# Kernel tuning notes

Hardware: AMD Instinct MI355X
Metric: run time of the kernel (lower is better)

The kernel has to match this reference:

```python
import jax, jax.numpy as jnp
import numpy as np

T, B, NIN = 256, 256, 512
NH, NEMB = 512, 256


def setup_inputs() -> dict:
    key = jax.random.key(0)
    ks = jax.random.split(key, 11)
    s = 0.02  # small init to keep tanh/sigmoid in active range
    return {
        "feats": jax.random.normal(ks[0], (T, B, NIN), jnp.float32),
        "h": jax.random.normal(ks[1], (B, NH), jnp.float32),
        "cur_embed": jax.random.normal(ks[2], (B, NEMB), jnp.float32),
        # i2h: Linear(nIn, nHidden, bias=False)
        "w_i2h": jax.random.normal(ks[3], (NH, NIN), jnp.float32) * s,
        # h2h: Linear(nHidden, nHidden) with bias
        "w_h2h": jax.random.normal(ks[4], (NH, NH), jnp.float32) * s,
        "b_h2h": jax.random.normal(ks[5], (NH,), jnp.float32) * s,
        # score: Linear(nHidden, 1, bias=False)
        "w_score": jax.random.normal(ks[6], (NH,), jnp.float32) * s,
        # GRUCell(nIn + num_embeddings, nHidden); gate order r, z, n
        "w_ih": jax.random.normal(ks[7], (3 * NH, NIN + NEMB), jnp.float32) * s,
        "w_hh": jax.random.normal(ks[8], (3 * NH, NH), jnp.float32) * s,
        "b_ih": jax.random.normal(ks[9], (3 * NH,), jnp.float32) * s,
        "b_hh": jax.random.normal(ks[10], (3 * NH,), jnp.float32) * s,
    }


def reference(feats, h, cur_embed, w_i2h, w_h2h, b_h2h, w_score,
              w_ih, w_hh, b_ih, b_hh):
    # MORAN branch, test=True (FractionalPickup is skipped at eval time).
    # feats: [T, B, nIn], h: [B, nHidden], cur_embed: [B, nEmb]
    feats_ = jnp.einsum('tbc,hc->tbh', feats, w_i2h)          # i2h, [T,B,H]
    h_ = h @ w_h2h.T + b_h2h                                   # h2h, [B,H]
    emit = jnp.einsum('tbh,h->tb', jnp.tanh(feats_ + h_[None]), w_score)
    alpha = jax.nn.softmax(emit, axis=0)                       # softmax over T
    context = jnp.einsum('tb,tbc->bc', alpha, feats)           # [B,nIn]
    x = jnp.concatenate([context, cur_embed], axis=1)          # [B,nIn+nEmb]
    # GRUCell
    gi = x @ w_ih.T + b_ih                                     # [B,3H]
    gh = h @ w_hh.T + b_hh                                     # [B,3H]
    gi_r, gi_z, gi_n = jnp.split(gi, 3, axis=1)
    gh_r, gh_z, gh_n = jnp.split(gh, 3, axis=1)
    r = jax.nn.sigmoid(gi_r + gh_r)
    z = jax.nn.sigmoid(gi_z + gh_z)
    n = jnp.tanh(gi_n + r * gh_n)
    nh = (1.0 - z) * n + z * h
    return nh, alpha
```

## Files before the change

kernel.cpp:

```cpp
#include <hip/hip_runtime.h>

typedef __bf16 bf16;
typedef __bf16 bf16x4 __attribute__((ext_vector_type(4)));
typedef __bf16 bf16x8 __attribute__((ext_vector_type(8)));
typedef float  f32x4  __attribute__((ext_vector_type(4)));

#define T_DIM 256
#define B_DIM 256
#define NIN   512
#define NH    512
#define NEMB  256
#define NX    768
#define NG    1536

__device__ __forceinline__ float fast_tanh(float x) {
    float e = __expf(2.0f * x);
    return 1.0f - 2.0f * __builtin_amdgcn_rcpf(e + 1.0f);
}
__device__ __forceinline__ float fast_sigmoid(float x) {
    return __builtin_amdgcn_rcpf(1.0f + __expf(-x));
}

__device__ __forceinline__ int swz(int rc) { return ((rc >> 1) & 3) << 3; }

__global__ __launch_bounds__(256) void cvt_weights(
    const float* __restrict__ a0, const float* __restrict__ a1,
    const float* __restrict__ a2, const float* __restrict__ a3,
    const float* __restrict__ a4,
    bf16* __restrict__ b0, bf16* __restrict__ b1, bf16* __restrict__ b2,
    bf16* __restrict__ b3, bf16* __restrict__ b4) {
    const int N0 = 65536, N1 = 131072, N2 = 425984, N3 = 622592, N4 = 655360;
    for (int i = blockIdx.x * 256 + threadIdx.x; i < N4; i += gridDim.x * 256) {
        const float* s; bf16* d; int j; bool img = false;
        if (i < N0)      { s = a0; d = b0; j = i; img = true; }
        else if (i < N1) { s = a1; d = b1; j = i - N0; }
        else if (i < N2) { s = a2; d = b2; j = i - N1; }
        else if (i < N3) { s = a3; d = b3; j = i - N2; }
        else             { s = a4; d = b4; j = i - N3; }
        float4 v = reinterpret_cast<const float4*>(s)[j];
        bf16x4 o = { (bf16)v.x, (bf16)v.y, (bf16)v.z, (bf16)v.w };
        if (img) {
            int e = j * 4, col = e >> 9, kc = e & 511, kk = kc >> 5, k = kc & 31;
            int off = kk * 16384 + col * 32 + (k ^ swz(col));
            *reinterpret_cast<bf16x4*>(d + off) = o;
        } else {
            reinterpret_cast<bf16x4*>(d)[j] = o;
        }
    }
}

__global__ __launch_bounds__(256) void gemm_bias(
    const bf16* __restrict__ A, const bf16* __restrict__ B,
    const float* __restrict__ bias, float* __restrict__ C,
    int M, int N, int K) {
    __shared__ bf16 At[64][40];
    __shared__ bf16 Bt[64][40];
    const int tid = threadIdx.x;
    const int m0 = blockIdx.y * 64, n0 = blockIdx.x * 64;
    const int wid = tid >> 6, lane = tid & 63, hi = lane >> 4, lo = lane & 15;
    const int srow = tid >> 2, sseg = tid & 3;
    f32x4 acc[4] = {};

    for (int kk = 0; kk < K; kk += 32) {
        bf16x8 av = *reinterpret_cast<const bf16x8*>(A + (size_t)(m0 + srow) * K + kk + sseg * 8);
        bf16x8 bv = *reinterpret_cast<const bf16x8*>(B + (size_t)(n0 + srow) * K + kk + sseg * 8);
        __syncthreads();
        *reinterpret_cast<bf16x8*>(&At[srow][sseg * 8]) = av;
        *reinterpret_cast<bf16x8*>(&Bt[srow][sseg * 8]) = bv;
        __syncthreads();
        bf16x8 a = *reinterpret_cast<const bf16x8*>(&At[wid * 16 + lo][hi * 8]);
#pragma unroll
        for (int nt = 0; nt < 4; ++nt) {
            bf16x8 b = *reinterpret_cast<const bf16x8*>(&Bt[nt * 16 + lo][hi * 8]);
            acc[nt] = __builtin_amdgcn_mfma_f32_16x16x32_bf16(a, b, acc[nt], 0, 0, 0);
        }
    }
#pragma unroll
    for (int nt = 0; nt < 4; ++nt) {
        int n = n0 + nt * 16 + lo;
        float bv = bias[n];
#pragma unroll
        for (int r = 0; r < 4; ++r) {
            int m = m0 + wid * 16 + hi * 4 + r;
            C[(size_t)m * N + n] = acc[nt][r] + bv;
        }
    }
}

__global__ __launch_bounds__(512, 2) void emit_kernel(
    const float* __restrict__ feats, const bf16* __restrict__ Wimg,
    const float* __restrict__ hbuf, const float* __restrict__ wscore,
    float* __restrict__ emit_out) {
    __shared__ bf16 Atile[2][2048];
    __shared__ float ew[512];
    const int tid = threadIdx.x;
    const int m0 = blockIdx.x * 64;
    const int wid = tid >> 6, lane = tid & 63, hi = lane >> 4, lo = lane & 15;

    const int arow = tid >> 3, akq = tid & 7;
    const int aoff = arow * 32 + ((akq * 4) ^ swz(arow));
    const float* asrc = feats + (size_t)(m0 + arow) * NIN + akq * 4;

    const int col0 = wid * 64 + lo;
    const bf16* bsrc = Wimg + col0 * 32 + ((hi * 8) ^ swz(col0));

    float4 fa[3];
    bf16x8 bfr[3][4];

    fa[0] = *reinterpret_cast<const float4*>(asrc);
    fa[1] = *reinterpret_cast<const float4*>(asrc + 32);
    fa[2] = *reinterpret_cast<const float4*>(asrc + 64);
#pragma unroll
    for (int s = 0; s < 2; ++s)
#pragma unroll
        for (int nt = 0; nt < 4; ++nt)
            bfr[s][nt] = *reinterpret_cast<const bf16x8*>(bsrc + s * 16384 + nt * 512);
    {
        bf16x4 o = { (bf16)fa[0].x, (bf16)fa[0].y, (bf16)fa[0].z, (bf16)fa[0].w };
        *reinterpret_cast<bf16x4*>(&Atile[0][aoff]) = o;
    }
    asm volatile("s_waitcnt lgkmcnt(0)" ::: "memory");
    __builtin_amdgcn_s_barrier();
    __builtin_amdgcn_sched_barrier(0);

    f32x4 acc[4][4] = {};
#pragma unroll
    for (int kk = 0; kk < 16; ++kk) {
        if (kk + 3 < 16)
            fa[kk % 3] = *reinterpret_cast<const float4*>(asrc + (kk + 3) * 32);
        if (kk + 2 < 16) {
#pragma unroll
            for (int nt = 0; nt < 4; ++nt)
                bfr[(kk + 2) % 3][nt] =
                    *reinterpret_cast<const bf16x8*>(bsrc + (kk + 2) * 16384 + nt * 512);
        }
        bf16x8 a[4];
#pragma unroll
        for (int st = 0; st < 4; ++st) {
            int row = st * 16 + lo;
            a[st] = *reinterpret_cast<const bf16x8*>(
                &Atile[kk & 1][row * 32 + ((hi * 8) ^ swz(row))]);
        }
#pragma unroll
        for (int nt = 0; nt < 4; ++nt)
#pragma unroll
            for (int st = 0; st < 4; ++st)
                acc[nt][st] = __builtin_amdgcn_mfma_f32_16x16x32_bf16(
                    a[st], bfr[kk % 3][nt], acc[nt][st], 0, 0, 0);
        if (kk + 1 < 16) {
            float4 f = fa[(kk + 1) % 3];
            bf16x4 o = { (bf16)f.x, (bf16)f.y, (bf16)f.z, (bf16)f.w };
            *reinterpret_cast<bf16x4*>(&Atile[(kk + 1) & 1][aoff]) = o;
            asm volatile("s_waitcnt lgkmcnt(0)" ::: "memory");
            __builtin_amdgcn_sched_barrier(0);
            __builtin_amdgcn_s_barrier();
            __builtin_amdgcn_sched_barrier(0);
        }
    }

    float ep[4][4] = {};
    const int bbase = m0 & (B_DIM - 1);
    const int n0 = wid * 64;
#pragma unroll
    for (int nt = 0; nt < 4; ++nt) {
        int n = n0 + nt * 16 + lo;
        float wsn = wscore[n];
#pragma unroll
        for (int st = 0; st < 4; ++st) {
#pragma unroll
            for (int r = 0; r < 4; ++r) {
                int b = bbase + st * 16 + hi * 4 + r;
                float x = acc[nt][st][r] + hbuf[(size_t)b * NH + n];
                ep[st][r] += fast_tanh(x) * wsn;
            }
        }
    }
#pragma unroll
    for (int st = 0; st < 4; ++st)
#pragma unroll
        for (int r = 0; r < 4; ++r)
#pragma unroll
            for (int off = 1; off < 16; off <<= 1)
                ep[st][r] += __shfl_xor(ep[st][r], off, 64);

    if (lo == 0) {
#pragma unroll
        for (int st = 0; st < 4; ++st)
#pragma unroll
            for (int r = 0; r < 4; ++r)
                ew[wid * 64 + st * 16 + hi * 4 + r] = ep[st][r];
    }
    __syncthreads();
    if (tid < 64) {
        float s = 0.0f;
#pragma unroll
        for (int ww = 0; ww < 8; ++ww) s += ew[ww * 64 + tid];
        emit_out[m0 + tid] = s;
    }
}

__global__ __launch_bounds__(256) void softmax_t(
    const float* __restrict__ emit, float* __restrict__ alpha, float* __restrict__ out_alpha) {
    int b = blockIdx.x, t = threadIdx.x;
    int wv = t >> 6, ln = t & 63;
    float e = emit[(size_t)t * B_DIM + b];
    float m = e;
#pragma unroll
    for (int off = 32; off; off >>= 1) m = fmaxf(m, __shfl_xor(m, off, 64));
    __shared__ float red[4], red2[4];
    if (ln == 0) red[wv] = m;
    __syncthreads();
    m = fmaxf(fmaxf(red[0], red[1]), fmaxf(red[2], red[3]));
    float p = __expf(e - m);
    float s = p;
#pragma unroll
    for (int off = 32; off; off >>= 1) s += __shfl_xor(s, off, 64);
    if (ln == 0) red2[wv] = s;
    __syncthreads();
    float inv = __builtin_amdgcn_rcpf(red2[0] + red2[1] + red2[2] + red2[3]);
    float a = p * inv;
    alpha[(size_t)t * B_DIM + b] = a;
    out_alpha[(size_t)t * B_DIM + b] = a;
}

__global__ __launch_bounds__(256) void ctx_kernel(
    const float* __restrict__ feats, const float* __restrict__ alpha,
    const float* __restrict__ emb, bf16* __restrict__ x) {
    int b = blockIdx.x;
    __shared__ float al[T_DIM];
    __shared__ float red[4][512];
    int tid = threadIdx.x;
    al[tid] = alpha[(size_t)tid * B_DIM + b];
    __syncthreads();
    int c8 = tid & 63, tq = tid >> 6;
    float acc[8] = {};
    for (int t = tq * 64; t < tq * 64 + 64; ++t) {
        const float* src = feats + ((size_t)(t * B_DIM + b)) * NIN + c8 * 8;
        float4 v0 = *reinterpret_cast<const float4*>(src);
        float4 v1 = *reinterpret_cast<const float4*>(src + 4);
        float a = al[t];
        acc[0] += a * v0.x; acc[1] += a * v0.y; acc[2] += a * v0.z; acc[3] += a * v0.w;
        acc[4] += a * v1.x; acc[5] += a * v1.y; acc[6] += a * v1.z; acc[7] += a * v1.w;
    }
#pragma unroll
    for (int j = 0; j < 8; ++j) red[tq][c8 * 8 + j] = acc[j];
    __syncthreads();
#pragma unroll
    for (int k = 0; k < 2; ++k) {
        int c = tid * 2 + k;
        float s = red[0][c] + red[1][c] + red[2][c] + red[3][c];
        x[(size_t)b * NX + c] = (bf16)s;
    }
    x[(size_t)b * NX + NIN + tid] = (bf16)emb[(size_t)b * NEMB + tid];
}

__global__ __launch_bounds__(256) void gru_kernel(
    const float* __restrict__ gi, const float* __restrict__ gh,
    const float* __restrict__ h, float* __restrict__ out) {
    int idx = blockIdx.x * 256 + threadIdx.x;
    int b = idx >> 9, j = idx & 511;
    const float* gib = gi + (size_t)b * NG;
    const float* ghb = gh + (size_t)b * NG;
    float r = fast_sigmoid(gib[j] + ghb[j]);
    float z = fast_sigmoid(gib[NH + j] + ghb[NH + j]);
    float n = fast_tanh(gib[2 * NH + j] + r * ghb[2 * NH + j]);
    out[idx] = (1.0f - z) * n + z * h[idx];
}

extern "C" void kernel_launch(void* const* d_in, const int* in_sizes, int n_in,
                              void* d_out, int out_size, void* d_ws, size_t ws_size,
                              hipStream_t stream) {
    const float* feats = (const float*)d_in[0];
    const float* h     = (const float*)d_in[1];
    const float* emb   = (const float*)d_in[2];
    const float* w_i2h = (const float*)d_in[3];
    const float* w_h2h = (const float*)d_in[4];
    const float* b_h2h = (const float*)d_in[5];
    const float* w_sc  = (const float*)d_in[6];
    const float* w_ih  = (const float*)d_in[7];
    const float* w_hh  = (const float*)d_in[8];
    const float* b_ih  = (const float*)d_in[9];
    const float* b_hh  = (const float*)d_in[10];
    float* out = (float*)d_out;

    char* ws = (char*)d_ws;
    bf16*  Wimg    = (bf16*)(ws);
    bf16*  w_h2h_b = (bf16*)(ws + 524288);
    bf16*  w_ih_b  = (bf16*)(ws + 1048576);
    bf16*  w_hh_b  = (bf16*)(ws + 3407872);
    bf16*  h_b     = (bf16*)(ws + 4980736);
    bf16*  x_b     = (bf16*)(ws + 5242880);
    float* hbuf    = (float*)(ws + 5636096);
    float* emit    = (float*)(ws + 6160384);
    float* alpha   = (float*)(ws + 6422528);
    float* gi      = (float*)(ws + 6684672);
    float* gh      = (float*)(ws + 8257536);

    cvt_weights<<<1024, 256, 0, stream>>>(w_i2h, w_h2h, w_ih, w_hh, h,
                                          Wimg, w_h2h_b, w_ih_b, w_hh_b, h_b);

    gemm_bias<<<dim3(8, 4), 256, 0, stream>>>(h_b, w_h2h_b, b_h2h, hbuf, 256, NH, NH);

    emit_kernel<<<1024, 512, 0, stream>>>(feats, Wimg, hbuf, w_sc, emit);

    softmax_t<<<256, 256, 0, stream>>>(emit, alpha, out + 131072);

    ctx_kernel<<<256, 256, 0, stream>>>(feats, alpha, emb, x_b);

    gemm_bias<<<dim3(24, 4), 256, 0, stream>>>(x_b, w_ih_b, b_ih, gi, 256, NG, NX);
    gemm_bias<<<dim3(24, 4), 256, 0, stream>>>(h_b, w_hh_b, b_hh, gh, 256, NG, NH);

    gru_kernel<<<512, 256, 0, stream>>>(gi, gh, h, out);
}
```

Baseline: 128.3 us.

## Stage full feats row tile in LDS upfront and drop per-step barriers in emit

The emit kernel now loads a block's entire 64x512 feats tile into LDS once, converting it to bf16 with a wider swizzle, then runs all 16 k-steps with no barriers. Only the weight fragments are double-buffered from global memory. The weight image loses its swizzle, and the launch bound requests 4 blocks per CU. The aim is to remove 15 barrier syncs per block and the tight register prefetch ring. In exchange it uses 64KB of LDS per block, which may prevent the requested occupancy, and it exposes the full feats load latency up front. The gh GEMM is also moved earlier in the launch order, which does not change dependencies.

```diff
diff --git a/kernel.cpp b/kernel.cpp
--- a/kernel.cpp
+++ b/kernel.cpp
@@ -21,7 +21,7 @@
     return __builtin_amdgcn_rcpf(1.0f + __expf(-x));
 }
 
-__device__ __forceinline__ int swz(int rc) { return ((rc >> 1) & 3) << 3; }
+__device__ __forceinline__ int swzk(int row) { return ((row >> 1) & 7) << 3; }
 
 __global__ __launch_bounds__(256) void cvt_weights(
     const float* __restrict__ a0, const float* __restrict__ a1,
@@ -41,8 +41,7 @@
         bf16x4 o = { (bf16)v.x, (bf16)v.y, (bf16)v.z, (bf16)v.w };
         if (img) {
             int e = j * 4, col = e >> 9, kc = e & 511, kk = kc >> 5, k = kc & 31;
-            int off = kk * 16384 + col * 32 + (k ^ swz(col));
-            *reinterpret_cast<bf16x4*>(d + off) = o;
+            *reinterpret_cast<bf16x4*>(d + kk * 16384 + col * 32 + k) = o;
         } else {
             reinterpret_cast<bf16x4*>(d)[j] = o;
         }
@@ -87,74 +86,56 @@
     }
 }
 
-__global__ __launch_bounds__(512, 2) void emit_kernel(
+__global__ __launch_bounds__(512, 4) void emit_kernel(
     const float* __restrict__ feats, const bf16* __restrict__ Wimg,
     const float* __restrict__ hbuf, const float* __restrict__ wscore,
     float* __restrict__ emit_out) {
-    __shared__ bf16 Atile[2][2048];
+    __shared__ bf16 Atile[64 * 512];
     __shared__ float ew[512];
     const int tid = threadIdx.x;
     const int m0 = blockIdx.x * 64;
     const int wid = tid >> 6, lane = tid & 63, hi = lane >> 4, lo = lane & 15;
 
-    const int arow = tid >> 3, akq = tid & 7;
-    const int aoff = arow * 32 + ((akq * 4) ^ swz(arow));
-    const float* asrc = feats + (size_t)(m0 + arow) * NIN + akq * 4;
+    const int arow = tid >> 3, aseg = tid & 7;
+    const float* asrc = feats + (size_t)(m0 + arow) * NIN + aseg * 4;
+    float4 va[16];
+#pragma unroll
+    for (int j = 0; j < 16; ++j)
+        va[j] = *reinterpret_cast<const float4*>(asrc + j * 32);
+#pragma unroll
+    for (int j = 0; j < 16; ++j) {
+        bf16x4 o = { (bf16)va[j].x, (bf16)va[j].y, (bf16)va[j].z, (bf16)va[j].w };
+        *reinterpret_cast<bf16x4*>(
+            &Atile[arow * 512 + ((j * 32 + aseg * 4) ^ swzk(arow))]) = o;
+    }
+    __syncthreads();
 
     const int col0 = wid * 64 + lo;
-    const bf16* bsrc = Wimg + col0 * 32 + ((hi * 8) ^ swz(col0));
-
-    float4 fa[3];
-    bf16x8 bfr[3][4];
-
-    fa[0] = *reinterpret_cast<const float4*>(asrc);
-    fa[1] = *reinterpret_cast<const float4*>(asrc + 32);
-    fa[2] = *reinterpret_cast<const float4*>(asrc + 64);
-#pragma unroll
-    for (int s = 0; s < 2; ++s)
-#pragma unroll
-        for (int nt = 0; nt < 4; ++nt)
-            bfr[s][nt] = *reinterpret_cast<const bf16x8*>(bsrc + s * 16384 + nt * 512);
-    {
-        bf16x4 o = { (bf16)fa[0].x, (bf16)fa[0].y, (bf16)fa[0].z, (bf16)fa[0].w };
-        *reinterpret_cast<bf16x4*>(&Atile[0][aoff]) = o;
-    }
-    asm volatile("s_waitcnt lgkmcnt(0)" ::: "memory");
-    __builtin_amdgcn_s_barrier();
-    __builtin_amdgcn_sched_barrier(0);
+    const bf16* bsrc = Wimg + col0 * 32 + hi * 8;
+    bf16x8 bb[2][4];
+#pragma unroll
+    for (int nt = 0; nt < 4; ++nt)
+        bb[0][nt] = *reinterpret_cast<const bf16x8*>(bsrc + nt * 512);
 
     f32x4 acc[4][4] = {};
 #pragma unroll
     for (int kk = 0; kk < 16; ++kk) {
-        if (kk + 3 < 16)
-            fa[kk % 3] = *reinterpret_cast<const float4*>(asrc + (kk + 3) * 32);
-        if (kk + 2 < 16) {
+        const int cur = kk & 1, nxt = cur ^ 1;
+        if (kk < 15) {
 #pragma unroll
             for (int nt = 0; nt < 4; ++nt)
-                bfr[(kk + 2) % 3][nt] =
-                    *reinterpret_cast<const bf16x8*>(bsrc + (kk + 2) * 16384 + nt * 512);
-        }
-        bf16x8 a[4];
+                bb[nxt][nt] = *reinterpret_cast<const bf16x8*>(
+                    bsrc + (kk + 1) * 16384 + nt * 512);
+        }
 #pragma unroll
         for (int st = 0; st < 4; ++st) {
-            int row = st * 16 + lo;
-            a[st] = *reinterpret_cast<const bf16x8*>(
-                &Atile[kk & 1][row * 32 + ((hi * 8) ^ swz(row))]);
-        }
-#pragma unroll
-        for (int nt = 0; nt < 4; ++nt)
-#pragma unroll
-            for (int st = 0; st < 4; ++st)
+            const int row = st * 16 + lo;
+            bf16x8 a = *reinterpret_cast<const bf16x8*>(
+                &Atile[row * 512 + ((kk * 32 + hi * 8) ^ swzk(row))]);
+#pragma unroll
+            for (int nt = 0; nt < 4; ++nt)
                 acc[nt][st] = __builtin_amdgcn_mfma_f32_16x16x32_bf16(
-                    a[st], bfr[kk % 3][nt], acc[nt][st], 0, 0, 0);
-        if (kk + 1 < 16) {
-            float4 f = fa[(kk + 1) % 3];
-            bf16x4 o = { (bf16)f.x, (bf16)f.y, (bf16)f.z, (bf16)f.w };
-            *reinterpret_cast<bf16x4*>(&Atile[(kk + 1) & 1][aoff]) = o;
-            asm volatile("s_waitcnt lgkmcnt(0)" ::: "memory");
-            __builtin_amdgcn_sched_barrier(0);
-            __builtin_amdgcn_s_barrier();
-            __builtin_amdgcn_sched_barrier(0);
+                    a, bb[cur][nt], acc[nt][st], 0, 0, 0);
         }
     }
 
@@ -300,6 +281,7 @@
                                           Wimg, w_h2h_b, w_ih_b, w_hh_b, h_b);
 
     gemm_bias<<<dim3(8, 4), 256, 0, stream>>>(h_b, w_h2h_b, b_h2h, hbuf, 256, NH, NH);
+    gemm_bias<<<dim3(24, 4), 256, 0, stream>>>(h_b, w_hh_b, b_hh, gh, 256, NG, NH);
 
     emit_kernel<<<1024, 512, 0, stream>>>(feats, Wimg, hbuf, w_sc, emit);
 
@@ -308,7 +290,6 @@
     ctx_kernel<<<256, 256, 0, stream>>>(feats, alpha, emb, x_b);
 
     gemm_bias<<<dim3(24, 4), 256, 0, stream>>>(x_b, w_ih_b, b_ih, gi, 256, NG, NX);
-    gemm_bias<<<dim3(24, 4), 256, 0, stream>>>(h_b, w_hh_b, b_hh, gh, 256, NG, NH);
 
     gru_kernel<<<512, 256, 0, stream>>>(gi, gh, h, out);
 }
```

Measured after the change: 133.5 us. +4.0%, slower.
